# Kernel tuning notes

Measured on AMD Instinct MI355X. Metric: run time of the kernel, lower is better.

Reference implementation:

```python
import jax, jax.numpy as jnp
import numpy as np

N, D, K = 10240, 256, 30  # nodes, feature dim, top-k
EPS = 1e-12  # F.normalize eps


def setup_inputs() -> dict:
    key = jax.random.key(0)
    k1, _ = jax.random.split(key)
    features = jax.random.normal(k1, (N, D), dtype=jnp.float32)
    # Attentive layers: elementwise feature weights, initialized to ones (as in the repo)
    w1 = jnp.ones((D,), dtype=jnp.float32)
    w2 = jnp.ones((D,), dtype=jnp.float32)
    return {"features": features, "w1": w1, "w2": w2, "k": K}


def reference(features, w1, w2, k):
    # internal_forward: Attentive = x * w (x @ diag(w)); relu between layers (mlp_act='relu')
    h = jax.nn.relu(features * w1) * w2              # [N, D]
    # F.normalize(dim=1, p=2) with eps clamp
    norm = jnp.maximum(jnp.linalg.norm(h, axis=1, keepdims=True), EPS)
    emb = h / norm                                   # [N, D]
    # cal_similarity_graph: dense cosine similarity
    sim = emb @ emb.T                                # [N, N]
    # top_k(sim, k+1): keep top (k+1) entries per row, zero the rest
    _, idx = jax.lax.top_k(sim, k + 1)               # [N, k+1]
    rows = jnp.arange(sim.shape[0])[:, None]
    mask = jnp.zeros_like(sim).at[rows, idx].set(1.0)
    # apply_non_linearity with 'relu'
    return jax.nn.relu(sim * mask)
```

## Files before the change

### kernel.cpp

```cpp
#include <hip/hip_runtime.h>
#include <math.h>

#define N_NODES 10240
#define DIM 256
#define TPB 256
#define CAP 1536
#define NB (N_NODES / 128)
#define NTRI (NB * (NB + 1) / 2)

typedef _Float16 half8 __attribute__((ext_vector_type(8)));
typedef float f32x4 __attribute__((ext_vector_type(4)));

__device__ __forceinline__ void async_load16(const void* g, void* l) {
  __builtin_amdgcn_global_load_lds(
      (const __attribute__((address_space(1))) unsigned int*)g,
      (__attribute__((address_space(3))) unsigned int*)l, 16, 0, 0);
}

__global__ __launch_bounds__(256) void norm_split_kernel(
    const float* __restrict__ F, const float* __restrict__ w1,
    const float* __restrict__ w2, _Float16* __restrict__ P0,
    _Float16* __restrict__ P1) {
  int row = blockIdx.x, tid = threadIdx.x;
  __shared__ float red[TPB];
  size_t base = (size_t)row * DIM + tid;
  float h = fmaxf(F[base] * w1[tid], 0.0f) * w2[tid];
  red[tid] = h * h;
  __syncthreads();
  for (int o = TPB / 2; o > 0; o >>= 1) {
    if (tid < o) red[tid] += red[tid + o];
    __syncthreads();
  }
  float e = h / fmaxf(sqrtf(red[0]), 1e-12f);
  _Float16 p0 = (_Float16)e;
  _Float16 p1 = (_Float16)((e - (float)p0) * 2048.0f);
  P0[base] = p0;
  P1[base] = p1;
}

__global__ __launch_bounds__(256) void gemm_mfma_kernel(
    const _Float16* __restrict__ P0, const _Float16* __restrict__ P1,
    float* __restrict__ C) {
  __shared__ char smem[32768];
  char* AsB = smem;
  char* BsB = smem + 16384;

  int tid = threadIdx.x;
  int lane = tid & 63;
  int w = tid >> 6;
  int wr = (w >> 1) * 64;
  int wc = (w & 1) * 64;
  int quad = lane >> 4;
  int mr = lane & 15;

  int t0 = blockIdx.x;
  int by;
  {
    float a = 2.0f * NB + 1.0f;
    float disc = a * a - 8.0f * (float)t0;
    by = (int)((a - sqrtf(disc)) * 0.5f);
    if (by > NB - 1) by = NB - 1;
    if (by < 0) by = 0;
    while (by > 0 && by * NB - (by * (by - 1)) / 2 > t0) --by;
    while (by < NB - 1 && (by + 1) * NB - ((by + 1) * by) / 2 <= t0) ++by;
  }
  int bx = by + (t0 - (by * NB - (by * (by - 1)) / 2));
  int rowBase = by * 128;
  int colBase = bx * 128;

  size_t rowOffA[4], rowOffB[4];
  int ldsOff[4];
#pragma unroll
  for (int i = 0; i < 4; ++i) {
    int u = tid + i * 256;
    int m = u >> 3;
    int g = (u & 7) ^ (m & 7);
    ldsOff[i] = u * 16;
    rowOffA[i] = (size_t)(rowBase + m) * DIM + g * 8;
    rowOffB[i] = (size_t)(colBase + m) * DIM + g * 8;
  }

  int fOffA[2][4], fOffB[2][4];
#pragma unroll
  for (int s = 0; s < 2; ++s)
#pragma unroll
    for (int t = 0; t < 4; ++t) {
      int g = s * 4 + quad;
      int mA = wr + t * 16 + mr;
      fOffA[s][t] = (mA * 8 + (g ^ (mA & 7))) * 16;
      int mB = wc + t * 16 + mr;
      fOffB[s][t] = (mB * 8 + (g ^ (mB & 7))) * 16;
    }

  f32x4 acc[4][4];
#pragma unroll
  for (int t = 0; t < 4; ++t)
#pragma unroll
    for (int u2 = 0; u2 < 4; ++u2) acc[t][u2] = (f32x4)0.0f;

  const _Float16* Aseg[3] = {P0, P1, P0};
  const _Float16* Bseg[3] = {P1, P0, P0};

  for (int pass = 0; pass < 3; ++pass) {
    if (pass == 2) {
      const float sc = 1.0f / 2048.0f;
#pragma unroll
      for (int t = 0; t < 4; ++t)
#pragma unroll
        for (int u2 = 0; u2 < 4; ++u2)
#pragma unroll
          for (int r = 0; r < 4; ++r) acc[t][u2][r] *= sc;
    }
    const _Float16* Ap = Aseg[pass];
    const _Float16* Bp = Bseg[pass];
    for (int c = 0; c < 4; ++c) {
      int kb = c * 64;
#pragma unroll
      for (int i = 0; i < 4; ++i)
        async_load16(Ap + rowOffA[i] + kb, AsB + ldsOff[i]);
#pragma unroll
      for (int i = 0; i < 4; ++i)
        async_load16(Bp + rowOffB[i] + kb, BsB + ldsOff[i]);
      __syncthreads();
#pragma unroll
      for (int s = 0; s < 2; ++s) {
        half8 af[4], bf[4];
#pragma unroll
        for (int t = 0; t < 4; ++t) {
          af[t] = *(const half8*)(AsB + fOffA[s][t]);
          bf[t] = *(const half8*)(BsB + fOffB[s][t]);
        }
#pragma unroll
        for (int t = 0; t < 4; ++t)
#pragma unroll
          for (int u2 = 0; u2 < 4; ++u2)
            acc[t][u2] = __builtin_amdgcn_mfma_f32_16x16x32_f16(
                af[t], bf[u2], acc[t][u2], 0, 0, 0);
      }
      __syncthreads();
    }
  }

#pragma unroll
  for (int t = 0; t < 4; ++t) {
    int gr = rowBase + wr + t * 16 + quad * 4;
#pragma unroll
    for (int u2 = 0; u2 < 4; ++u2) {
      int gc = colBase + wc + u2 * 16 + mr;
      float* cp = C + (size_t)gr * N_NODES + gc;
      cp[0] = acc[t][u2][0];
      cp[(size_t)N_NODES] = acc[t][u2][1];
      cp[(size_t)2 * N_NODES] = acc[t][u2][2];
      cp[(size_t)3 * N_NODES] = acc[t][u2][3];
    }
  }
  if (bx != by) {
#pragma unroll
    for (int t = 0; t < 4; ++t) {
      int gr = rowBase + wr + t * 16 + quad * 4;
#pragma unroll
      for (int u2 = 0; u2 < 4; ++u2) {
        int gc = colBase + wc + u2 * 16 + mr;
        *(f32x4*)(C + (size_t)gc * N_NODES + gr) = acc[t][u2];
      }
    }
  }
}

__global__ __launch_bounds__(256) void topk_kernel(
    float* __restrict__ C, const int* __restrict__ kptr) {
  constexpr int EPT = N_NODES / TPB;
  constexpr int NV4 = EPT / 4;
  __shared__ unsigned int lm[TPB];
  __shared__ unsigned int cu[CAP];
  __shared__ int ci[CAP];
  __shared__ unsigned int s_cnt, s_L31, s_Tu;
  __shared__ int s_Jcut;

  int tid = threadIdx.x;
  float* Crow = C + (size_t)blockIdx.x * N_NODES;
  unsigned int want = (unsigned int)(kptr[0] + 1);

  unsigned int u[EPT];
  unsigned int lmax = 0u;
#pragma unroll
  for (int i = 0; i < NV4; ++i) {
    float4 v = *(const float4*)&Crow[(i * TPB + tid) * 4];
    float fv[4] = {v.x, v.y, v.z, v.w};
#pragma unroll
    for (int c = 0; c < 4; ++c) {
      unsigned int s = __float_as_uint(fv[c]);
      unsigned int m = (s & 0x80000000u) ? ~s : (s | 0x80000000u);
      u[i * 4 + c] = m;
      lmax = (m > lmax) ? m : lmax;
    }
  }
  lm[tid] = lmax;
  if (tid == 0) s_cnt = 0u;
  __syncthreads();

  {
    unsigned int r = 0;
    for (int j = 0; j < TPB; ++j) {
      unsigned int vj = lm[j];
      r += (vj > lmax) || (vj == lmax && j < tid);
    }
    if (r == want - 1) s_L31 = lmax;
  }
  __syncthreads();
  unsigned int L31 = s_L31;

#pragma unroll
  for (int i = 0; i < EPT; ++i) {
    if (u[i] >= L31) {
      unsigned int pos = atomicAdd(&s_cnt, 1u);
      if (pos < CAP) {
        cu[pos] = u[i];
        ci[pos] = ((i / 4) * TPB + tid) * 4 + (i % 4);
      }
    }
  }
  __syncthreads();
  unsigned int c_total = s_cnt;

  if (c_total <= CAP) {
    for (unsigned int i = tid; i < c_total; i += TPB) {
      unsigned int ui = cu[i];
      int ii = ci[i];
      unsigned int r = 0;
      for (unsigned int j = 0; j < c_total; ++j) {
        unsigned int uj = cu[j];
        r += (uj > ui) || (uj == ui && ci[j] < ii);
      }
      if (r == want - 1) { s_Tu = ui; s_Jcut = ii; }
    }
    __syncthreads();
  } else {
    unsigned int lo = 0u, hi = 0xFFFFFFFFu;
    while (lo < hi) {
      unsigned int mid = lo + ((hi - lo) >> 1);
      unsigned int cnt = 0;
#pragma unroll
      for (int i = 0; i < EPT; ++i) cnt += (u[i] > mid) ? 1u : 0u;
      lm[tid] = cnt;
      __syncthreads();
      for (int o = TPB / 2; o > 0; o >>= 1) {
        if (tid < o) lm[tid] += lm[tid + o];
        __syncthreads();
      }
      unsigned int gcnt = lm[0];
      __syncthreads();
      if (gcnt < want) hi = mid; else lo = mid + 1u;
    }
    unsigned int Tu = lo;
    unsigned int cnt = 0;
#pragma unroll
    for (int i = 0; i < EPT; ++i) cnt += (u[i] > Tu) ? 1u : 0u;
    lm[tid] = cnt;
    __syncthreads();
    for (int o = TPB / 2; o > 0; o >>= 1) {
      if (tid < o) lm[tid] += lm[tid + o];
      __syncthreads();
    }
    unsigned int need = want - lm[0];
    __syncthreads();
    int jlo = 0, jhi = N_NODES - 1;
    while (jlo < jhi) {
      int jmid = (jlo + jhi) >> 1;
      unsigned int cc = 0;
#pragma unroll
      for (int i = 0; i < EPT; ++i) {
        int jj = ((i / 4) * TPB + tid) * 4 + (i % 4);
        cc += (u[i] == Tu && jj <= jmid) ? 1u : 0u;
      }
      lm[tid] = cc;
      __syncthreads();
      for (int o = TPB / 2; o > 0; o >>= 1) {
        if (tid < o) lm[tid] += lm[tid + o];
        __syncthreads();
      }
      unsigned int tot = lm[0];
      __syncthreads();
      if (tot >= need) jhi = jmid; else jlo = jmid + 1;
    }
    if (tid == 0) { s_Tu = Tu; s_Jcut = jlo; }
    __syncthreads();
  }

  unsigned int Tu = s_Tu;
  int Jcut = s_Jcut;

#pragma unroll
  for (int i = 0; i < NV4; ++i) {
    float out[4];
#pragma unroll
    for (int c = 0; c < 4; ++c) {
      unsigned int m = u[i * 4 + c];
      int j = (i * TPB + tid) * 4 + c;
      bool keep = (m > Tu) || (m == Tu && j <= Jcut);
      float v = __uint_as_float((m & 0x80000000u) ? (m ^ 0x80000000u) : ~m);
      out[c] = (keep && v > 0.0f) ? v : 0.0f;
    }
    *(float4*)&Crow[(i * TPB + tid) * 4] =
        make_float4(out[0], out[1], out[2], out[3]);
  }
}

extern "C" void kernel_launch(void* const* d_in, const int* in_sizes, int n_in,
                              void* d_out, int out_size, void* d_ws, size_t ws_size,
                              hipStream_t stream) {
  const float* F  = (const float*)d_in[0];
  const float* w1 = (const float*)d_in[1];
  const float* w2 = (const float*)d_in[2];
  const int*   kp = (const int*)d_in[3];
  float* C = (float*)d_out;
  _Float16* P0 = (_Float16*)d_ws;
  _Float16* P1 = P0 + (size_t)N_NODES * DIM;

  norm_split_kernel<<<N_NODES, DIM, 0, stream>>>(F, w1, w2, P0, P1);

  gemm_mfma_kernel<<<NTRI, 256, 0, stream>>>(P0, P1, C);

  topk_kernel<<<N_NODES, TPB, 0, stream>>>(C, kp);
}
```

Baseline: 674.7 us.

## Stage transposed GEMM tile writes through LDS and vectorize top-k rank loops

The mirrored (transposed) tile store in the symmetric GEMM now goes through shared memory in four 32-column chunks, so each row of C is written with coalesced 16-byte stores instead of scattered column writes. The float-sqrt triangular index decode is replaced with a simple subtraction loop. In the top-k kernel, the rank-counting loops over the LDS max array and the candidate array read 4 elements per load using uint4/int4, with padding sentinels added to the candidate array. The changes add extra barriers and LDS traffic in the GEMM epilogue in exchange for coalesced global writes.

```diff
diff --git a/kernel.cpp b/kernel.cpp
--- a/kernel.cpp
+++ b/kernel.cpp
@@ -41,7 +41,7 @@
 __global__ __launch_bounds__(256) void gemm_mfma_kernel(
     const _Float16* __restrict__ P0, const _Float16* __restrict__ P1,
     float* __restrict__ C) {
-  __shared__ char smem[32768];
+  __shared__ __align__(16) char smem[32768];
   char* AsB = smem;
   char* BsB = smem + 16384;
 
@@ -53,18 +53,9 @@
   int quad = lane >> 4;
   int mr = lane & 15;
 
-  int t0 = blockIdx.x;
-  int by;
-  {
-    float a = 2.0f * NB + 1.0f;
-    float disc = a * a - 8.0f * (float)t0;
-    by = (int)((a - sqrtf(disc)) * 0.5f);
-    if (by > NB - 1) by = NB - 1;
-    if (by < 0) by = 0;
-    while (by > 0 && by * NB - (by * (by - 1)) / 2 > t0) --by;
-    while (by < NB - 1 && (by + 1) * NB - ((by + 1) * by) / 2 <= t0) ++by;
-  }
-  int bx = by + (t0 - (by * NB - (by * (by - 1)) / 2));
+  int by = 0, rem = blockIdx.x;
+  while (rem >= NB - by) { rem -= NB - by; ++by; }
+  int bx = by + rem;
   int rowBase = by * 128;
   int colBase = bx * 128;
 
@@ -154,14 +145,33 @@
       cp[(size_t)3 * N_NODES] = acc[t][u2][3];
     }
   }
+
   if (bx != by) {
-#pragma unroll
-    for (int t = 0; t < 4; ++t) {
-      int gr = rowBase + wr + t * 16 + quad * 4;
-#pragma unroll
-      for (int u2 = 0; u2 < 4; ++u2) {
-        int gc = colBase + wc + u2 * 16 + mr;
-        *(f32x4*)(C + (size_t)gc * N_NODES + gr) = acc[t][u2];
+    float* Tr = (float*)smem;
+    for (int ch = 0; ch < 4; ++ch) {
+      __syncthreads();
+      if ((w & 1) == (ch >> 1)) {
+        int u2base = (ch & 1) * 2;
+#pragma unroll
+        for (int uu = 0; uu < 2; ++uu) {
+          int u2 = u2base + uu;
+          int jloc = uu * 16 + mr;
+#pragma unroll
+          for (int t = 0; t < 4; ++t) {
+            int i0 = wr + t * 16 + quad * 4;
+            *(f32x4*)&Tr[jloc * 132 + i0] = acc[t][u2];
+          }
+        }
+      }
+      __syncthreads();
+#pragma unroll
+      for (int p = 0; p < 4; ++p) {
+        int idx = tid + p * 256;
+        int row = idx >> 5;
+        int c4 = idx & 31;
+        f32x4 v = *(const f32x4*)&Tr[row * 132 + c4 * 4];
+        *(f32x4*)(C + (size_t)(colBase + ch * 32 + row) * N_NODES +
+                  rowBase + c4 * 4) = v;
       }
     }
   }
@@ -171,9 +181,9 @@
     float* __restrict__ C, const int* __restrict__ kptr) {
   constexpr int EPT = N_NODES / TPB;
   constexpr int NV4 = EPT / 4;
-  __shared__ unsigned int lm[TPB];
-  __shared__ unsigned int cu[CAP];
-  __shared__ int ci[CAP];
+  __shared__ __align__(16) unsigned int lm[TPB];
+  __shared__ __align__(16) unsigned int cu[CAP + 4];
+  __shared__ __align__(16) int ci[CAP + 4];
   __shared__ unsigned int s_cnt, s_L31, s_Tu;
   __shared__ int s_Jcut;
 
@@ -201,9 +211,15 @@
 
   {
     unsigned int r = 0;
-    for (int j = 0; j < TPB; ++j) {
-      unsigned int vj = lm[j];
-      r += (vj > lmax) || (vj == lmax && j < tid);
+    const uint4* lm4 = (const uint4*)lm;
+#pragma unroll 8
+    for (int jv = 0; jv < TPB / 4; ++jv) {
+      uint4 vj = lm4[jv];
+      int j0 = jv * 4;
+      r += (vj.x > lmax) || (vj.x == lmax && (j0 + 0) < tid);
+      r += (vj.y > lmax) || (vj.y == lmax && (j0 + 1) < tid);
+      r += (vj.z > lmax) || (vj.z == lmax && (j0 + 2) < tid);
+      r += (vj.w > lmax) || (vj.w == lmax && (j0 + 3) < tid);
     }
     if (r == want - 1) s_L31 = lmax;
   }
@@ -224,13 +240,25 @@
   unsigned int c_total = s_cnt;
 
   if (c_total <= CAP) {
+    unsigned int cpad = (c_total + 3u) & ~3u;
+    if (tid < (int)(cpad - c_total)) {
+      cu[c_total + tid] = 0u;
+      ci[c_total + tid] = 0x7FFFFFFF;
+    }
+    __syncthreads();
+    const uint4* cu4 = (const uint4*)cu;
+    const int4* ci4 = (const int4*)ci;
     for (unsigned int i = tid; i < c_total; i += TPB) {
       unsigned int ui = cu[i];
       int ii = ci[i];
       unsigned int r = 0;
-      for (unsigned int j = 0; j < c_total; ++j) {
-        unsigned int uj = cu[j];
-        r += (uj > ui) || (uj == ui && ci[j] < ii);
+      for (unsigned int jv = 0; jv < (cpad >> 2); ++jv) {
+        uint4 uj = cu4[jv];
+        int4 ij = ci4[jv];
+        r += (uj.x > ui) || (uj.x == ui && ij.x < ii);
+        r += (uj.y > ui) || (uj.y == ui && ij.y < ii);
+        r += (uj.z > ui) || (uj.z == ui && ij.z < ii);
+        r += (uj.w > ui) || (uj.w == ui && ij.w < ii);
       }
       if (r == want - 1) { s_Tu = ui; s_Jcut = ii; }
     }
```

New measurement: 720.2 us. +6.7%, slower.
